# Kernel optimization log

Measured on AMD Instinct MI355X. Metric: run time of the kernel, lower is better.

Reference implementation:

```python
import jax, jax.numpy as jnp
import numpy as np

B, C = 2, 2
D = H = W = 192
N_BIF = 64                 # bif ids 0..63; labels = bif*4 + stub (stub in 1..3)
NUM_LABELS = 4 * N_BIF     # 256
MIN_STUBS = 2
MIN_VOXELS = 1
TEMP = 0.2


def setup_inputs() -> dict:
    key = jax.random.key(0)
    k1, k2 = jax.random.split(key)
    pred = jax.random.normal(k1, (B, C, D, H, W), dtype=jnp.float32)
    stub_label_map = jax.random.randint(k2, (B, 1, D, H, W), 0, NUM_LABELS).astype(jnp.float32)
    return {"pred": pred, "stub_label_map": stub_label_map}


def reference(pred, stub_label_map):
    # foreground probability: softmax over channel dim, take class 1
    fg = jax.nn.softmax(pred, axis=1)[:, 1]                     # [B,D,H,W]
    labels = jnp.round(stub_label_map[:, 0]).astype(jnp.int32)  # [B,D,H,W]

    Bn = fg.shape[0]
    fg_flat = fg.reshape(Bn, -1)
    lab_flat = labels.reshape(Bn, -1)

    seg = lambda v, i: jax.ops.segment_sum(v, i, num_segments=NUM_LABELS)
    sums = jax.vmap(seg)(fg_flat, lab_flat)                      # [B, NUM_LABELS]
    counts = jax.vmap(seg)(jnp.ones_like(fg_flat), lab_flat)     # [B, NUM_LABELS]

    # group labels as [bif, stub]; drop bif 0 and stub 0 (never used in loop)
    sums = sums.reshape(Bn, N_BIF, 4)[:, 1:, 1:4]                # [B, N_BIF-1, 3]
    counts = counts.reshape(Bn, N_BIF, 4)[:, 1:, 1:4]

    valid = counts >= MIN_VOXELS                                 # stub has enough voxels
    means = sums / jnp.maximum(counts, 1.0)                      # per-stub mean fg prob

    # softmin over the valid stubs of each bif (masked softmax of -mean/temp)
    logits = jnp.where(valid, -means / TEMP, -1e9)
    weights = jax.nn.softmax(logits, axis=-1)
    score = jnp.sum(jnp.where(valid, means * weights, 0.0), axis=-1)  # [B, N_BIF-1]

    valid_bif = jnp.sum(valid, axis=-1) >= MIN_STUBS
    total = jnp.sum(jnp.where(valid_bif, 1.0 - score, 0.0))
    n_bifs = jnp.sum(valid_bif)
    return jnp.where(n_bifs > 0, total / jnp.maximum(n_bifs, 1).astype(total.dtype), 0.0)
```

## Files before the change

kernel.cpp:

```cpp
#include <hip/hip_runtime.h>
#include <math.h>

#define BATCH     2
#define NLAB      256
#define VOX       (192*192*192)
#define TEMP      0.2f
#define GRIDX     768
#define NITER     ((VOX/4)/(GRIDX*256))
#define STRIDE    (GRIDX*256)
#define NPART     16

#define STEP      4096.0f
#define INV_STEP  (1.0f/4096.0f)

typedef unsigned int u32;
typedef __attribute__((ext_vector_type(8))) short bf16x8;
typedef __attribute__((ext_vector_type(4))) float f32x4;
union FragU { uint4 u; bf16x8 v; };

__device__ __forceinline__ u32 fgbf16(float pa, float pc) {
    const float fg = __builtin_amdgcn_rcpf(1.0f + __expf(pa - pc));
    u32 bits = __float_as_uint(fg);
    bits += 0x7FFFu + ((bits >> 16) & 1u);
    return bits >> 16;
}

__device__ __forceinline__ void voxmask(float pl, u32& hm, u32& lmm) {
    const u32 lab = ((u32)(int)(pl + 0.5f)) & 255u;
    hm  = 1u << (lab >> 4);
    lmm = 1u << (lab & 15u);
}

#define PAIRH(whi, wlo, fp, aw, b1w, b2w) do {                              \
    const u32 _h = ((whi) >> mlane) & 0x10001u;                             \
    const u32 _l = ((wlo) >> mlane) & 0x10001u;                             \
    aw  = __umul24(_h, 0x3F80u);                                            \
    b1w = __umul24(_l, 0x3F80u);                                            \
    b2w = (fp) & __umul24(_l, 0xFFFFu);                                     \
} while (0)

#define PACKIT(av, cv, lv, WHIA, WLOA, WHIB, WLOB, FGA, FGB) do {           \
    u32 hm0, lm0, hm1, lm1, hm2, lm2, hm3, lm3;                             \
    voxmask((lv).x, hm0, lm0);                                              \
    voxmask((lv).y, hm1, lm1);                                              \
    voxmask((lv).z, hm2, lm2);                                              \
    voxmask((lv).w, hm3, lm3);                                              \
    WHIA = hm0 | (hm1 << 16);                                               \
    WLOA = lm0 | (lm1 << 16);                                               \
    WHIB = hm2 | (hm3 << 16);                                               \
    WLOB = lm2 | (lm3 << 16);                                               \
    FGA  = fgbf16((av).x, (cv).x) | (fgbf16((av).y, (cv).y) << 16);         \
    FGB  = fgbf16((av).z, (cv).z) | (fgbf16((av).w, (cv).w) << 16);         \
} while (0)

__global__ __launch_bounds__(256, 6) void histo_kernel(
    const float* __restrict__ pred,
    const float* __restrict__ labmap,
    float* __restrict__ ws_slots)
{
    __shared__ __align__(16) u32 s_iv[4][2][256];
    __shared__ __align__(16) u32 s_fg[4][2][128];

    const int b    = blockIdx.y;
    const int tid  = threadIdx.x;
    const int w    = tid >> 6;
    const int lane = tid & 63;
    const u32 mlane = (u32)(lane & 15);
    const int g    = lane >> 4;

    const float4* p0 = (const float4*)(pred + (size_t)b * 2 * VOX);
    const float4* p1 = (const float4*)(pred + (size_t)b * 2 * VOX + VOX);
    const float4* lm = (const float4*)(labmap + (size_t)b * VOX);

    f32x4 accC = {0.f, 0.f, 0.f, 0.f};
    f32x4 accS = {0.f, 0.f, 0.f, 0.f};

    const int base = blockIdx.x * 256 + tid;

    {
        const float4 a0 = p0[base], c0 = p1[base], l0 = lm[base];
        u32 whiA, wloA, whiB, wloB, fgA, fgB;
        PACKIT(a0, c0, l0, whiA, wloA, whiB, wloB, fgA, fgB);
        *(uint4*)(&s_iv[w][0][0] + (lane << 2)) =
            make_uint4(whiA, wloA, whiB, wloB);
        *(uint2*)(&s_fg[w][0][0] + (lane << 1)) = make_uint2(fgA, fgB);
    }
    float4 a1 = p0[base + STRIDE], c1 = p1[base + STRIDE], l1 = lm[base + STRIDE];

    for (int it = 0; it < NITER; ++it) {
        if (it + 1 < NITER) {
            u32 whiA, wloA, whiB, wloB, fgA, fgB;
            PACKIT(a1, c1, l1, whiA, wloA, whiB, wloB, fgA, fgB);
            u32* iv  = &s_iv[w][(it + 1) & 1][0];
            u32* fgp = &s_fg[w][(it + 1) & 1][0];
            *(uint4*)(iv + (lane << 2)) = make_uint4(whiA, wloA, whiB, wloB);
            *(uint2*)(fgp + (lane << 1)) = make_uint2(fgA, fgB);
        }
        {
            const int nit = (it + 2 < NITER) ? (it + 2) : (NITER - 1);
            const int inx = base + nit * STRIDE;
            a1 = p0[inx]; c1 = p1[inx]; l1 = lm[inx];
        }

        const u32* rp = &s_iv[w][it & 1][0] + (g << 3);
        const u32* rf = &s_fg[w][it & 1][0] + (g << 2);

        uint4 q0 = *(const uint4*)(rp);
        uint4 q1 = *(const uint4*)(rp + 4);
        uint4 fq = *(const uint4*)(rf);
        #pragma unroll
        for (int t = 0; t < 8; ++t) {
            uint4 q0n, q1n, fqn;
            if (t < 7) {
                q0n = *(const uint4*)(rp + (t + 1) * 32);
                q1n = *(const uint4*)(rp + (t + 1) * 32 + 4);
                fqn = *(const uint4*)(rf + (t + 1) * 16);
            }
            u32 a0, a1w, a2, a3, b10, b11, b12, b13, b20, b21, b22, b23;
            PAIRH(q0.x, q0.y, fq.x, a0,  b10, b20);
            PAIRH(q0.z, q0.w, fq.y, a1w, b11, b21);
            PAIRH(q1.x, q1.y, fq.z, a2,  b12, b22);
            PAIRH(q1.z, q1.w, fq.w, a3,  b13, b23);
            FragU A, B1, B2;
            A.u  = make_uint4(a0, a1w, a2, a3);
            B1.u = make_uint4(b10, b11, b12, b13);
            B2.u = make_uint4(b20, b21, b22, b23);
            accC = __builtin_amdgcn_mfma_f32_16x16x32_bf16(A.v, B1.v, accC, 0, 0, 0);
            accS = __builtin_amdgcn_mfma_f32_16x16x32_bf16(A.v, B2.v, accS, 0, 0, 0);
            if (t < 7) { q0 = q0n; q1 = q1n; fq = fqn; }
        }
    }

    float* cnt_w = (float*)&s_iv[w][0][0];
    float* sum_w = (float*)&s_iv[w][1][0];
    const int row0 = (lane >> 4) << 2;
    const int colb = lane & 15;
    #pragma unroll
    for (int j = 0; j < 4; ++j) {
        cnt_w[(row0 + j) * 16 + colb] = accC[j];
        sum_w[(row0 + j) * 16 + colb] = accS[j];
    }
    __syncthreads();

    float cs = 0.0f, ss = 0.0f;
    #pragma unroll
    for (int ww = 0; ww < 4; ++ww) {
        cs += ((float*)&s_iv[ww][0][0])[tid];
        ss += ((float*)&s_iv[ww][1][0])[tid];
    }
    ws_slots[((size_t)(b * GRIDX + blockIdx.x)) * NLAB + tid] = ss + STEP * cs;
}

__global__ __launch_bounds__(256) void reduce_kernel(
    const float* __restrict__ ws_slots,
    float* __restrict__ psum,
    float* __restrict__ pcnt)
{
    const int bin  = threadIdx.x;
    const int b    = blockIdx.x / NPART;
    const int part = blockIdx.x % NPART;
    const int per  = GRIDX / NPART;

    float cs = 0.0f, ss = 0.0f;
    for (int s = part * per; s < (part + 1) * per; ++s) {
        float v = ws_slots[((size_t)(b * GRIDX + s)) * NLAB + bin];
        float c = floorf(v * INV_STEP + 0.5f);
        cs += c;
        ss += v - c * STEP;
    }
    psum[(size_t)blockIdx.x * NLAB + bin] = ss;
    pcnt[(size_t)blockIdx.x * NLAB + bin] = cs;
}

__global__ __launch_bounds__(256) void scalar_kernel(
    const float* __restrict__ psum,
    const float* __restrict__ pcnt,
    float* __restrict__ out)
{
    __shared__ float s_fsum[BATCH][NLAB];
    __shared__ float s_fcnt[BATCH][NLAB];

    const int tid = threadIdx.x;

    for (int b = 0; b < BATCH; ++b) {
        float ss = 0.0f, cs = 0.0f;
        for (int p = 0; p < NPART; ++p) {
            ss += psum[(size_t)(b * NPART + p) * NLAB + tid];
            cs += pcnt[(size_t)(b * NPART + p) * NLAB + tid];
        }
        s_fsum[b][tid] = ss;
        s_fcnt[b][tid] = cs;
    }
    __syncthreads();

    if (tid < 64) {
        float total = 0.0f;
        float nbifs = 0.0f;
        if (tid >= 1) {
            for (int bb = 0; bb < BATCH; ++bb) {
                float means[3];
                bool  valid[3];
                int   nvalid = 0;
                for (int s = 0; s < 3; ++s) {
                    int lab = tid * 4 + 1 + s;
                    float cnt = s_fcnt[bb][lab];
                    float sum = s_fsum[bb][lab];
                    valid[s] = (cnt >= 1.0f);
                    means[s] = sum / fmaxf(cnt, 1.0f);
                    nvalid  += valid[s] ? 1 : 0;
                }
                float logits[3], m = -3e38f;
                for (int s = 0; s < 3; ++s) {
                    logits[s] = valid[s] ? (-means[s] / TEMP) : -1e9f;
                    m = fmaxf(m, logits[s]);
                }
                float e[3], se = 0.0f;
                for (int s = 0; s < 3; ++s) { e[s] = __expf(logits[s] - m); se += e[s]; }
                float score = 0.0f;
                for (int s = 0; s < 3; ++s) {
                    if (valid[s]) score += means[s] * (e[s] / se);
                }
                if (nvalid >= 2) {
                    total += 1.0f - score;
                    nbifs += 1.0f;
                }
            }
        }
        for (int off = 32; off > 0; off >>= 1) {
            total += __shfl_down(total, off);
            nbifs += __shfl_down(nbifs, off);
        }
        if (tid == 0) {
            out[0] = (nbifs > 0.0f) ? (total / fmaxf(nbifs, 1.0f)) : 0.0f;
        }
    }
}

extern "C" void kernel_launch(void* const* d_in, const int* in_sizes, int n_in,
                              void* d_out, int out_size, void* d_ws, size_t ws_size,
                              hipStream_t stream) {
    const float* pred = (const float*)d_in[0];
    const float* lab  = (const float*)d_in[1];

    float* ws_slots = (float*)d_ws;
    float* psum = ws_slots + (size_t)BATCH * GRIDX * NLAB;
    float* pcnt = psum + (size_t)BATCH * NPART * NLAB;

    dim3 grid(GRIDX, BATCH);
    histo_kernel<<<grid, 256, 0, stream>>>(pred, lab, ws_slots);
    reduce_kernel<<<BATCH * NPART, 256, 0, stream>>>(ws_slots, psum, pcnt);
    scalar_kernel<<<1, 256, 0, stream>>>(psum, pcnt, (float*)d_out);
}
```

Measured before the change: 212.6 us.

## Hand-schedule LDS reads with inline asm and a triple-buffered waitcnt pipeline

After: 207.5 us. -2.4%, faster.

```diff
diff --git a/kernel.cpp b/kernel.cpp
--- a/kernel.cpp
+++ b/kernel.cpp
@@ -14,9 +14,11 @@
 #define INV_STEP  (1.0f/4096.0f)
 
 typedef unsigned int u32;
+typedef __attribute__((ext_vector_type(2))) u32 u32x2;
+typedef __attribute__((ext_vector_type(4))) u32 u32x4;
 typedef __attribute__((ext_vector_type(8))) short bf16x8;
 typedef __attribute__((ext_vector_type(4))) float f32x4;
-union FragU { uint4 u; bf16x8 v; };
+union FragU { u32x4 u; bf16x8 v; };
 
 __device__ __forceinline__ u32 fgbf16(float pa, float pc) {
     const float fg = __builtin_amdgcn_rcpf(1.0f + __expf(pa - pc));
@@ -53,6 +55,33 @@
     FGB  = fgbf16((av).z, (cv).z) | (fgbf16((av).w, (cv).w) << 16);         \
 } while (0)
 
+#define TILE_ISSUE(T, Q0, Q1, FQ)                                           \
+    asm volatile("ds_read_b128 %0, %3 offset:%c5\n\t"                       \
+                 "ds_read_b128 %1, %3 offset:%c6\n\t"                       \
+                 "ds_read_b128 %2, %4 offset:%c7"                           \
+                 : "=&v"(Q0), "=&v"(Q1), "=&v"(FQ)                          \
+                 : "v"(amask), "v"(afg),                                    \
+                   "i"((T)*128), "i"((T)*128 + 16), "i"((T)*64))
+
+#define WAITL(N) do {                                                       \
+    asm volatile("s_waitcnt lgkmcnt(%c0)" :: "i"(N));                       \
+    __builtin_amdgcn_sched_barrier(0);                                      \
+} while (0)
+
+#define TILE_BUILD(Q0, Q1, FQ) do {                                         \
+    u32 a0, a1w, a2, a3, b10, b11, b12, b13, b20, b21, b22, b23;            \
+    PAIRH((Q0).x, (Q0).y, (FQ).x, a0,  b10, b20);                           \
+    PAIRH((Q0).z, (Q0).w, (FQ).y, a1w, b11, b21);                           \
+    PAIRH((Q1).x, (Q1).y, (FQ).z, a2,  b12, b22);                           \
+    PAIRH((Q1).z, (Q1).w, (FQ).w, a3,  b13, b23);                           \
+    FragU A, B1, B2;                                                        \
+    A.u  = (u32x4){a0, a1w, a2, a3};                                        \
+    B1.u = (u32x4){b10, b11, b12, b13};                                     \
+    B2.u = (u32x4){b20, b21, b22, b23};                                     \
+    accC = __builtin_amdgcn_mfma_f32_16x16x32_bf16(A.v, B1.v, accC, 0,0,0); \
+    accS = __builtin_amdgcn_mfma_f32_16x16x32_bf16(A.v, B2.v, accS, 0,0,0); \
+} while (0)
+
 __global__ __launch_bounds__(256, 6) void histo_kernel(
     const float* __restrict__ pred,
     const float* __restrict__ labmap,
@@ -77,58 +106,40 @@
 
     const int base = blockIdx.x * 256 + tid;
 
-    {
-        const float4 a0 = p0[base], c0 = p1[base], l0 = lm[base];
-        u32 whiA, wloA, whiB, wloB, fgA, fgB;
-        PACKIT(a0, c0, l0, whiA, wloA, whiB, wloB, fgA, fgB);
-        *(uint4*)(&s_iv[w][0][0] + (lane << 2)) =
-            make_uint4(whiA, wloA, whiB, wloB);
-        *(uint2*)(&s_fg[w][0][0] + (lane << 1)) = make_uint2(fgA, fgB);
-    }
-    float4 a1 = p0[base + STRIDE], c1 = p1[base + STRIDE], l1 = lm[base + STRIDE];
+    float4 a = p0[base], c = p1[base], l = lm[base];
 
     for (int it = 0; it < NITER; ++it) {
-        if (it + 1 < NITER) {
+        const int nit = (it + 1 < NITER) ? (it + 1) : it;
+        const int inx = base + nit * STRIDE;
+        const float4 an = p0[inx], cn = p1[inx], ln = lm[inx];
+
+        {
             u32 whiA, wloA, whiB, wloB, fgA, fgB;
-            PACKIT(a1, c1, l1, whiA, wloA, whiB, wloB, fgA, fgB);
-            u32* iv  = &s_iv[w][(it + 1) & 1][0];
-            u32* fgp = &s_fg[w][(it + 1) & 1][0];
-            *(uint4*)(iv + (lane << 2)) = make_uint4(whiA, wloA, whiB, wloB);
-            *(uint2*)(fgp + (lane << 1)) = make_uint2(fgA, fgB);
-        }
-        {
-            const int nit = (it + 2 < NITER) ? (it + 2) : (NITER - 1);
-            const int inx = base + nit * STRIDE;
-            a1 = p0[inx]; c1 = p1[inx]; l1 = lm[inx];
-        }
-
-        const u32* rp = &s_iv[w][it & 1][0] + (g << 3);
-        const u32* rf = &s_fg[w][it & 1][0] + (g << 2);
-
-        uint4 q0 = *(const uint4*)(rp);
-        uint4 q1 = *(const uint4*)(rp + 4);
-        uint4 fq = *(const uint4*)(rf);
-        #pragma unroll
-        for (int t = 0; t < 8; ++t) {
-            uint4 q0n, q1n, fqn;
-            if (t < 7) {
-                q0n = *(const uint4*)(rp + (t + 1) * 32);
-                q1n = *(const uint4*)(rp + (t + 1) * 32 + 4);
-                fqn = *(const uint4*)(rf + (t + 1) * 16);
-            }
-            u32 a0, a1w, a2, a3, b10, b11, b12, b13, b20, b21, b22, b23;
-            PAIRH(q0.x, q0.y, fq.x, a0,  b10, b20);
-            PAIRH(q0.z, q0.w, fq.y, a1w, b11, b21);
-            PAIRH(q1.x, q1.y, fq.z, a2,  b12, b22);
-            PAIRH(q1.z, q1.w, fq.w, a3,  b13, b23);
-            FragU A, B1, B2;
-            A.u  = make_uint4(a0, a1w, a2, a3);
-            B1.u = make_uint4(b10, b11, b12, b13);
-            B2.u = make_uint4(b20, b21, b22, b23);
-            accC = __builtin_amdgcn_mfma_f32_16x16x32_bf16(A.v, B1.v, accC, 0, 0, 0);
-            accS = __builtin_amdgcn_mfma_f32_16x16x32_bf16(A.v, B2.v, accS, 0, 0, 0);
-            if (t < 7) { q0 = q0n; q1 = q1n; fq = fqn; }
-        }
+            PACKIT(a, c, l, whiA, wloA, whiB, wloB, fgA, fgB);
+            u32* iv  = &s_iv[w][it & 1][0];
+            u32* fgp = &s_fg[w][it & 1][0];
+            *(u32x4*)(iv + (lane << 2))  = (u32x4){whiA, wloA, whiB, wloB};
+            *(u32x2*)(fgp + (lane << 1)) = (u32x2){fgA, fgB};
+        }
+        asm volatile("" ::: "memory");
+
+        const u32 amask = (u32)(size_t)&s_iv[w][it & 1][0] + 32u * (u32)g;
+        const u32 afg   = (u32)(size_t)&s_fg[w][it & 1][0] + 16u * (u32)g;
+
+        u32x4 qA0, qA1, fA, qB0, qB1, fB, qC0, qC1, fC;
+        TILE_ISSUE(0, qA0, qA1, fA);
+        TILE_ISSUE(1, qB0, qB1, fB);
+        TILE_ISSUE(2, qC0, qC1, fC);
+        WAITL(6); TILE_BUILD(qA0, qA1, fA); TILE_ISSUE(3, qA0, qA1, fA);
+        WAITL(6); TILE_BUILD(qB0, qB1, fB); TILE_ISSUE(4, qB0, qB1, fB);
+        WAITL(6); TILE_BUILD(qC0, qC1, fC); TILE_ISSUE(5, qC0, qC1, fC);
+        WAITL(6); TILE_BUILD(qA0, qA1, fA); TILE_ISSUE(6, qA0, qA1, fA);
+        WAITL(6); TILE_BUILD(qB0, qB1, fB); TILE_ISSUE(7, qB0, qB1, fB);
+        WAITL(6); TILE_BUILD(qC0, qC1, fC);
+        WAITL(3); TILE_BUILD(qA0, qA1, fA);
+        WAITL(0); TILE_BUILD(qB0, qB1, fB);
+
+        a = an; c = cn; l = ln;
     }
 
     float* cnt_w = (float*)&s_iv[w][0][0];
```
